# Performance work log

Hardware: AMD Instinct MI355X
Metric: run time of the kernel (lower is better)

Reference implementation:

```python
import jax, jax.numpy as jnp
import numpy as np
from jax import lax

C = 384          # input_dim
HEADS = 12       # num_heads_sp = max(1, 384*1.0 // 30)
HD = 32          # head_dim_sp = 384 // 12
NK = 3           # num_keys (full=True)
ATT_K, ATT_S = 7, 4
UP_K, UP_P = 8, 2   # ConvTranspose2d(kernel=att_stride*2, stride=4, padding=att_stride//2)
EPS = 1e-5
DN = ('NCHW', 'OIHW', 'NCHW')


def _gn(x, g, b):
    # GroupNorm(num_groups=1): normalize over (C,H,W) per sample, per-channel affine
    mu = jnp.mean(x, axis=(1, 2, 3), keepdims=True)
    var = jnp.var(x, axis=(1, 2, 3), keepdims=True)
    return (x - mu) * lax.rsqrt(var + EPS) * g[None, :, None, None] + b[None, :, None, None]


def _pw(x, w):
    # 1x1 conv as einsum; w: [out_ch, in_ch]
    return jnp.einsum('nchw,oc->nohw', x, w)


def _forward(x, dw_w, bn_gamma, bn_beta, bn_mean, bn_var, lnch_gamma, lnch_beta,
             pwise_ch_w, outch_w, outch_b, lnsp_gamma, lnsp_beta,
             pwise_sp_w, outsp_w, outsp_b, up_w, up_b):
    # depthwise strided downsampling conv + BatchNorm (eval mode)
    p = ATT_K // 2
    x_down = lax.conv_general_dilated(x, dw_w, (ATT_S, ATT_S), [(p, p), (p, p)],
                                      dimension_numbers=DN, feature_group_count=C)
    s = bn_gamma * lax.rsqrt(bn_var + EPS)
    x_down = x_down * s[None, :, None, None] + (bn_beta - bn_mean * s)[None, :, None, None]
    N, _, H, W = x_down.shape
    L = H * W
    # --- channel attention: tokens are channels, d_k = H*W ---
    qkv = _pw(_gn(x_down, lnch_gamma, lnch_beta), pwise_ch_w).reshape(N, NK * C, L)
    q, k, v = jnp.split(qkv, NK, axis=1)  # each [N, C, L]
    att = jax.nn.softmax(jnp.einsum('ncl,ndl->ncd', q, k) / jnp.sqrt(jnp.float32(L)), axis=-1)
    vals = jnp.einsum('ncd,ndl->ncl', att, v).reshape(N, C, H, W)
    x_down = x_down + _pw(vals, outch_w) + outch_b[None, :, None, None]
    # --- spatial multi-head attention over the H*W tokens ---
    qkv = _pw(_gn(x_down, lnsp_gamma, lnsp_beta), pwise_sp_w)
    qkv = qkv.reshape(N, HEADS, NK * HD, L).transpose(0, 1, 3, 2)  # [N,h,L,3*hd]
    q, k, v = jnp.split(qkv, NK, axis=-1)  # each [N,h,L,hd]
    att = jax.nn.softmax(jnp.einsum('nhld,nhmd->nhlm', q, k) / jnp.sqrt(jnp.float32(HD)), axis=-1)
    vals = jnp.einsum('nhlm,nhmd->nhld', att, v).transpose(0, 1, 3, 2).reshape(N, HEADS * HD, H, W)
    x_down = x_down + _pw(vals, outsp_w) + outsp_b[None, :, None, None]
    # --- depthwise transposed-conv upsampling (as lhs-dilated conv w/ flipped kernel) ---
    tp = UP_K - 1 - UP_P
    o = lax.conv_general_dilated(x_down, up_w[:, :, ::-1, ::-1], (1, 1), [(tp, tp), (tp, tp)],
                                 lhs_dilation=(ATT_S, ATT_S), dimension_numbers=DN,
                                 feature_group_count=C)
    return x + o + up_b[None, :, None, None]


def setup_inputs():
    key = jax.random.key(0)
    ks = jax.random.split(key, 8)
    w = lambda k, shp: jax.random.normal(k, shp, dtype=jnp.float32) * 0.05
    return {
        'x': jax.random.normal(ks[0], (16, C, 64, 64), dtype=jnp.float32),
        'dw_w': w(ks[1], (C, 1, ATT_K, ATT_K)),
        'bn_gamma': jnp.ones((C,), jnp.float32),
        'bn_beta': jnp.zeros((C,), jnp.float32),
        'bn_mean': jnp.zeros((C,), jnp.float32),
        'bn_var': jnp.ones((C,), jnp.float32),
        'lnch_gamma': jnp.ones((C,), jnp.float32),
        'lnch_beta': jnp.zeros((C,), jnp.float32),
        'pwise_ch_w': w(ks[2], (NK * C, C)),
        'outch_w': w(ks[3], (C, C)),
        'outch_b': jnp.zeros((C,), jnp.float32),
        'lnsp_gamma': jnp.ones((C,), jnp.float32),
        'lnsp_beta': jnp.zeros((C,), jnp.float32),
        'pwise_sp_w': w(ks[4], (NK * HEADS * HD, C)),
        'outsp_w': w(ks[5], (C, HEADS * HD)),
        'outsp_b': jnp.zeros((C,), jnp.float32),
        'up_w': w(ks[6], (C, 1, UP_K, UP_K)),
        'up_b': jnp.zeros((C,), jnp.float32),
    }


def reference(x, dw_w, bn_gamma, bn_beta, bn_mean, bn_var, lnch_gamma, lnch_beta,
              pwise_ch_w, outch_w, outch_b, lnsp_gamma, lnsp_beta,
              pwise_sp_w, outsp_w, outsp_b, up_w, up_b):
    return _forward(x, dw_w, bn_gamma, bn_beta, bn_mean, bn_var, lnch_gamma, lnch_beta,
                    pwise_ch_w, outch_w, outch_b, lnsp_gamma, lnsp_beta,
                    pwise_sp_w, outsp_w, outsp_b, up_w, up_b)
```

## Files before the change

### kernel.cpp

```cpp
#include <hip/hip_runtime.h>
#include <hip/hip_bf16.h>
#include <math.h>

typedef __hip_bfloat16 bf16;

#define NB  16
#define CCH 384
#define LDIM 256

typedef __attribute__((ext_vector_type(8))) short bh8;
typedef __attribute__((ext_vector_type(4))) float fx4;

__device__ __forceinline__ float ldin(const void* p, long i, bool f) {
    if (f) return ((const float*)p)[i];
    return __bfloat162float(((const bf16*)p)[i]);
}
__device__ __forceinline__ float b2f(unsigned short u) {
    union { unsigned short s; bf16 b; } c; c.s = u; return __bfloat162float(c.b);
}
__device__ __forceinline__ unsigned short f2b(float v) {
    bf16 h = __float2bfloat16(v);
    union { bf16 b; unsigned short s; } c; c.b = h; return c.s;
}
__device__ __forceinline__ float fin(float v, float marker) {
    return (v == v && fabsf(v) < 1e30f) ? v : marker;
}

__global__ void k_detect(const unsigned* __restrict__ g, int* __restrict__ flag) {
    if (threadIdx.x == 0) *flag = (*g == 0x3F800000u) ? 1 : 0;
}
__global__ void k_zero(float* __restrict__ p) { p[threadIdx.x] = 0.f; }

__global__ void k_dwconv_bn(const void* __restrict__ x, const void* __restrict__ w,
                            const void* __restrict__ gamma, const void* __restrict__ beta,
                            const void* __restrict__ mean, const void* __restrict__ var,
                            const int* __restrict__ flag, float* __restrict__ xd)
{
    bool f = *flag != 0;
    int c = blockIdx.x, n = blockIdx.y, t = threadIdx.x;
    int i = t >> 4, j = t & 15;
    float s = ldin(gamma, c, f) * rsqrtf(ldin(var, c, f) + 1e-5f);
    float bias = ldin(beta, c, f) - ldin(mean, c, f) * s;
    long xbase = (long)(n * CCH + c) << 12;
    float acc = 0.f;
    #pragma unroll
    for (int a = 0; a < 7; a++) {
        int yy = 4 * i + a - 3;
        if (yy < 0 || yy >= 64) continue;
        #pragma unroll
        for (int b = 0; b < 7; b++) {
            int xx = 4 * j + b - 3;
            if (xx < 0 || xx >= 64) continue;
            acc += ldin(x, xbase + (yy << 6) + xx, f) * ldin(w, c * 49 + a * 7 + b, f);
        }
    }
    xd[((long)(n * CCH + c) << 8) + t] = fin(acc * s + bias, 1.0e4f);
}

__global__ void k_gn_stats(const float* __restrict__ xd, float* __restrict__ stats)
{
    int n = blockIdx.y;
    const float* p = xd + (long)n * (CCH * LDIM) + blockIdx.x * 4096;
    float s = 0.f, s2 = 0.f;
    for (int i = threadIdx.x; i < 4096; i += 256) {
        float v = p[i];
        s += v; s2 += v * v;
    }
    #pragma unroll
    for (int o = 32; o; o >>= 1) { s += __shfl_down(s, o); s2 += __shfl_down(s2, o); }
    __shared__ float sh[4], sh2[4];
    int wid = threadIdx.x >> 6, lane = threadIdx.x & 63;
    if (lane == 0) { sh[wid] = s; sh2[wid] = s2; }
    __syncthreads();
    if (threadIdx.x == 0) {
        atomicAdd(&stats[n * 2],     sh[0] + sh[1] + sh[2] + sh[3]);
        atomicAdd(&stats[n * 2 + 1], sh2[0] + sh2[1] + sh2[2] + sh2[3]);
    }
}

template<bool TB, bool ACCUM, bool AIN, bool GNB>
__global__ __launch_bounds__(256) void k_gemm(
    const void* __restrict__ A, const float* __restrict__ B, float* __restrict__ Cm,
    const void* __restrict__ bias, const int* __restrict__ flag,
    const float* __restrict__ gnstats, const void* __restrict__ gng, const void* __restrict__ gnbt,
    int M, int N, int K, int lda, int ldb, int ldc, long sA, long sB, long sC, float alpha)
{
    bool f = *flag != 0;
    __shared__ unsigned short As[128 * 40];
    __shared__ unsigned short Bs[128 * 40];
    long aoff = (long)blockIdx.z * sA;
    const float* Bb = B + (long)blockIdx.z * sB;
    float* Cb = Cm + (long)blockIdx.z * sC;
    float mu = 0.f, rs = 0.f;
    if (GNB) {
        float S = gnstats[2 * blockIdx.z], S2 = gnstats[2 * blockIdx.z + 1];
        mu = S * (1.f / 98304.f);
        float var = S2 * (1.f / 98304.f) - mu * mu;
        rs = rsqrtf(fmaxf(var, 0.f) + 1e-5f);
    }
    int m0 = blockIdx.y << 7, n0 = blockIdx.x << 7;
    int t = threadIdx.x;
    int w = t >> 6, lane = t & 63;
    int wm = w >> 1, wn = w & 1;
    int lr = lane & 15, lg = lane >> 4;
    int amloc = t >> 3, akloc = (t & 7) << 2;
    int nloc = t & 127, ph = t >> 7;
    fx4 acc[4][4] = {};

    for (int k0 = 0; k0 < K; k0 += 32) {
        #pragma unroll
        for (int p = 0; p < 4; p++) {
            int m = (p << 5) + amloc;
            long ai = aoff + (long)(m0 + m) * lda + k0 + akloc;
            ushort4 uv;
            if (AIN && !f) {
                uv = *(const ushort4*)((const unsigned short*)A + ai);
            } else {
                float4 fv = *(const float4*)((const float*)A + ai);
                uv.x = f2b(fv.x); uv.y = f2b(fv.y); uv.z = f2b(fv.z); uv.w = f2b(fv.w);
            }
            *(ushort4*)&As[m * 40 + akloc] = uv;
        }
        if (!TB) {
            const float* Bp = Bb + n0 + nloc;
            #pragma unroll
            for (int i = 0; i < 8; i++) {
                int p = ph + (i << 1);
                int k = k0 + (p << 1);
                float v0 = Bp[(long)k * ldb];
                float v1 = Bp[(long)(k + 1) * ldb];
                if (GNB) {
                    v0 = (v0 - mu) * rs * ldin(gng, k, f) + ldin(gnbt, k, f);
                    v1 = (v1 - mu) * rs * ldin(gng, k + 1, f) + ldin(gnbt, k + 1, f);
                }
                unsigned int pk = (unsigned)f2b(v0) | ((unsigned)f2b(v1) << 16);
                *(unsigned int*)&Bs[nloc * 40 + (p << 1)] = pk;
            }
        } else {
            #pragma unroll
            for (int p = 0; p < 4; p++) {
                int n = (p << 5) + amloc;
                float4 fv = *(const float4*)(Bb + (long)(n0 + n) * ldb + k0 + akloc);
                ushort4 uv;
                uv.x = f2b(fv.x); uv.y = f2b(fv.y); uv.z = f2b(fv.z); uv.w = f2b(fv.w);
                *(ushort4*)&Bs[n * 40 + akloc] = uv;
            }
        }
        __syncthreads();
        bh8 a[4], b[4];
        #pragma unroll
        for (int mi = 0; mi < 4; mi++)
            a[mi] = *(const bh8*)&As[((wm << 6) + (mi << 4) + lr) * 40 + (lg << 3)];
        #pragma unroll
        for (int nj = 0; nj < 4; nj++)
            b[nj] = *(const bh8*)&Bs[((wn << 6) + (nj << 4) + lr) * 40 + (lg << 3)];
        #pragma unroll
        for (int mi = 0; mi < 4; mi++)
            #pragma unroll
            for (int nj = 0; nj < 4; nj++)
                acc[mi][nj] = __builtin_amdgcn_mfma_f32_16x16x32_bf16(a[mi], b[nj], acc[mi][nj], 0, 0, 0);
        __syncthreads();
    }
    #pragma unroll
    for (int mi = 0; mi < 4; mi++) {
        #pragma unroll
        for (int r = 0; r < 4; r++) {
            int m = m0 + (wm << 6) + (mi << 4) + (lg << 2) + r;
            float bv = bias ? ldin(bias, m, f) : 0.f;
            #pragma unroll
            for (int nj = 0; nj < 4; nj++) {
                int n = n0 + (wn << 6) + (nj << 4) + lr;
                long idx = (long)m * ldc + n;
                float v = alpha * acc[mi][nj][r] + bv;
                if (ACCUM) v += Cb[idx];
                Cb[idx] = fin(v, 4.0e4f);
            }
        }
    }
}

__global__ void k_softmax(float* __restrict__ a, int D)
{
    long row = blockIdx.x;
    float* p = a + row * D;
    int t = threadIdx.x;
    float m = -1e30f;
    for (int i = t; i < D; i += 256) m = fmaxf(m, p[i]);
    #pragma unroll
    for (int o = 32; o; o >>= 1) m = fmaxf(m, __shfl_down(m, o));
    __shared__ float shm[4], shs[4];
    int wid = t >> 6, lane = t & 63;
    if (lane == 0) shm[wid] = m;
    __syncthreads();
    m = fmaxf(fmaxf(shm[0], shm[1]), fmaxf(shm[2], shm[3]));
    float s = 0.f;
    for (int i = t; i < D; i += 256) {
        float e = __expf(p[i] - m);
        p[i] = e;
        s += e;
    }
    #pragma unroll
    for (int o = 32; o; o >>= 1) s += __shfl_down(s, o);
    if (lane == 0) shs[wid] = s;
    __syncthreads();
    float inv = 1.f / (shs[0] + shs[1] + shs[2] + shs[3]);
    for (int i = t; i < D; i += 256) p[i] *= inv;
}

__global__ __launch_bounds__(256) void k_spatt(const float* __restrict__ qkv,
                                               float* __restrict__ vals)
{
    __shared__ float Ks[256 * 36];
    __shared__ float Vs[256 * 36];
    int h = blockIdx.x, n = blockIdx.y, t = threadIdx.x;
    const float* base = qkv + (long)n * 294912 + h * 96 * 256;
    float q[32];
    #pragma unroll
    for (int i = 0; i < 32; i++) {
        q[i] = base[i * 256 + t];
        Ks[t * 36 + i] = base[(32 + i) * 256 + t];
        Vs[t * 36 + i] = base[(64 + i) * 256 + t];
    }
    __syncthreads();
    float o[32] = {};
    float mx = -1e30f, sum = 0.f;
    for (int m = 0; m < 256; m++) {
        float s = 0.f;
        #pragma unroll
        for (int i = 0; i < 8; i++) {
            float4 kv = *(const float4*)&Ks[m * 36 + 4 * i];
            s += q[4*i] * kv.x + q[4*i+1] * kv.y + q[4*i+2] * kv.z + q[4*i+3] * kv.w;
        }
        s *= 0.17677669529663687f;
        if (s > mx) {
            float c = __expf(mx - s);
            sum *= c;
            #pragma unroll
            for (int d = 0; d < 32; d++) o[d] *= c;
            mx = s;
        }
        float p = __expf(s - mx);
        sum += p;
        #pragma unroll
        for (int i = 0; i < 8; i++) {
            float4 vv = *(const float4*)&Vs[m * 36 + 4 * i];
            o[4*i] += p * vv.x; o[4*i+1] += p * vv.y; o[4*i+2] += p * vv.z; o[4*i+3] += p * vv.w;
        }
    }
    float inv = 1.f / sum;
    long ob = (long)n * 98304 + h * 8192;
    #pragma unroll
    for (int d = 0; d < 32; d++) vals[ob + d * 256 + t] = fin(o[d] * inv, 5.0e4f);
}

__global__ void k_upsample(const void* __restrict__ x, const float* __restrict__ xd,
                           const void* __restrict__ w, const void* __restrict__ ub,
                           const int* __restrict__ flag, void* __restrict__ out)
{
    bool f = *flag != 0;
    int c = blockIdx.y, n = blockIdx.z;
    int t = threadIdx.x;
    int p0 = (blockIdx.x * 256 + t) * 4;
    int y = p0 >> 6, xx0 = p0 & 63;
    const float* xdp = xd + ((long)(n * CCH + c) << 8);
    long base = (long)(n * CCH + c) << 12;
    float bias = ldin(ub, c, f);
    float acc[4];
    if (f) {
        #pragma unroll
        for (int e = 0; e < 4; e++) acc[e] = ((const float*)x)[base + p0 + e] + bias;
    } else {
        ushort4 xv = *(const ushort4*)((const unsigned short*)x + base + p0);
        acc[0] = b2f(xv.x) + bias; acc[1] = b2f(xv.y) + bias;
        acc[2] = b2f(xv.z) + bias; acc[3] = b2f(xv.w) + bias;
    }
    int ry = (y + 2) & 3;
    #pragma unroll
    for (int dy = 0; dy < 2; dy++) {
        int ky = ry + 4 * dy;
        int iy = (y + 2 - ky) >> 2;
        if (iy < 0 || iy >= 16) continue;
        #pragma unroll
        for (int e = 0; e < 4; e++) {
            int xxe = xx0 + e;
            int rx = (xxe + 2) & 3;
            #pragma unroll
            for (int dx = 0; dx < 2; dx++) {
                int kx = rx + 4 * dx;
                int ix = (xxe + 2 - kx) >> 2;
                if (ix < 0 || ix >= 16) continue;
                acc[e] += xdp[(iy << 4) + ix] * ldin(w, (c << 6) + (ky << 3) + kx, f);
            }
        }
    }
    if (f) {
        #pragma unroll
        for (int e = 0; e < 4; e++) ((float*)out)[base + p0 + e] = fin(acc[e], 9.0e4f);
    } else {
        ushort4 ov;
        ov.x = f2b(fin(acc[0], 9.0e4f)); ov.y = f2b(fin(acc[1], 9.0e4f));
        ov.z = f2b(fin(acc[2], 9.0e4f)); ov.w = f2b(fin(acc[3], 9.0e4f));
        *(ushort4*)((unsigned short*)out + base + p0) = ov;
    }
}

extern "C" void kernel_launch(void* const* d_in, const int* in_sizes, int n_in,
                              void* d_out, int out_size, void* d_ws, size_t ws_size,
                              hipStream_t stream)
{
    const void* x       = d_in[0];
    const void* dw_w    = d_in[1];
    const void* bn_g    = d_in[2];
    const void* bn_b    = d_in[3];
    const void* bn_m    = d_in[4];
    const void* bn_v    = d_in[5];
    const void* lnch_g  = d_in[6];
    const void* lnch_b  = d_in[7];
    const void* w_ch    = d_in[8];
    const void* outch_w = d_in[9];
    const void* outch_b = d_in[10];
    const void* lnsp_g  = d_in[11];
    const void* lnsp_b  = d_in[12];
    const void* w_sp    = d_in[13];
    const void* outsp_w = d_in[14];
    const void* outsp_b = d_in[15];
    const void* up_w    = d_in[16];
    const void* up_b    = d_in[17];
    float* ws = (float*)d_ws;

    float* xd    = ws;
    float* stats = ws + 1572864;
    int*   flag  = (int*)(ws + 1572864 + 32);

    float* ob   = (float*)d_out;
    float* vals = ob;
    float* qkv  = ob + 1572864;
    float* attb = qkv + 4718592;

    k_detect<<<1, 64, 0, stream>>>((const unsigned*)bn_g, flag);

    k_dwconv_bn<<<dim3(CCH, NB), 256, 0, stream>>>(x, dw_w, bn_g, bn_b, bn_m, bn_v, flag, xd);
    k_zero<<<1, 32, 0, stream>>>(stats);
    k_gn_stats<<<dim3(24, NB), 256, 0, stream>>>(xd, stats);
    k_gemm<false, false, true, true><<<dim3(2, 9, NB), 256, 0, stream>>>(
        w_ch, xd, qkv, nullptr, flag, stats, lnch_g, lnch_b,
        1152, 256, 384, 384, 256, 256, 0L, 98304L, 294912L, 1.f);
    k_gemm<true, false, false, false><<<dim3(3, 3, NB), 256, 0, stream>>>(
        qkv, qkv + 98304, attb, nullptr, flag, nullptr, nullptr, nullptr,
        384, 384, 256, 256, 256, 384, 294912L, 294912L, 147456L, 0.0625f);
    k_softmax<<<NB * 384, 256, 0, stream>>>(attb, 384);
    k_gemm<false, false, false, false><<<dim3(2, 3, NB), 256, 0, stream>>>(
        attb, qkv + 196608, vals, nullptr, flag, nullptr, nullptr, nullptr,
        384, 256, 384, 384, 256, 256, 147456L, 294912L, 98304L, 1.f);
    k_gemm<false, true, true, false><<<dim3(2, 3, NB), 256, 0, stream>>>(
        outch_w, vals, xd, outch_b, flag, nullptr, nullptr, nullptr,
        384, 256, 384, 384, 256, 256, 0L, 98304L, 98304L, 1.f);
    k_zero<<<1, 32, 0, stream>>>(stats);
    k_gn_stats<<<dim3(24, NB), 256, 0, stream>>>(xd, stats);
    k_gemm<false, false, true, true><<<dim3(2, 9, NB), 256, 0, stream>>>(
        w_sp, xd, qkv, nullptr, flag, stats, lnsp_g, lnsp_b,
        1152, 256, 384, 384, 256, 256, 0L, 98304L, 294912L, 1.f);
    k_spatt<<<dim3(12, NB), 256, 0, stream>>>(qkv, vals);
    k_gemm<false, true, true, false><<<dim3(2, 3, NB), 256, 0, stream>>>(
        outsp_w, vals, xd, outsp_b, flag, nullptr, nullptr, nullptr,
        384, 256, 384, 384, 256, 256, 0L, 98304L, 98304L, 1.f);
    k_upsample<<<dim3(4, CCH, NB), 256, 0, stream>>>(x, xd, up_w, up_b, flag, d_out);
}
```

Before: 650.8 us.

## Rewrite spatial attention with bf16 MFMA for QK^T and PV

Replaces the scalar per-thread online-softmax spatial attention with a two-stage matrix-core version. Q, K and V are converted to bf16 in shared memory, QK^T runs on 16x16x32 bf16 MFMAs, and a full-row softmax writes bf16 probabilities to swizzled shared memory. A second MFMA pass computes PV, and the output is transposed through shared memory for coalesced stores. It uses about 150KB of shared memory, which limits it to one block per CU, and lowers the precision of Q, K, V and the probabilities to bf16.

```diff
diff --git a/kernel.cpp b/kernel.cpp
--- a/kernel.cpp
+++ b/kernel.cpp
@@ -207,50 +207,131 @@
     for (int i = t; i < D; i += 256) p[i] *= inv;
 }
 
-__global__ __launch_bounds__(256) void k_spatt(const float* __restrict__ qkv,
-                                               float* __restrict__ vals)
-{
-    __shared__ float Ks[256 * 36];
-    __shared__ float Vs[256 * 36];
+__global__ __launch_bounds__(256, 1) void k_spatt(const float* __restrict__ qkv,
+                                                  float* __restrict__ vals)
+{
+    __shared__ __align__(16) unsigned char smem[152064];
+    unsigned short* Qs = (unsigned short*)smem;
+    unsigned short* Ks = (unsigned short*)(smem + 20480);
+    unsigned char*  Ps = smem;
+    unsigned char*  Vs = smem + 135168;
+    float*          Os = (float*)smem;
+
     int h = blockIdx.x, n = blockIdx.y, t = threadIdx.x;
     const float* base = qkv + (long)n * 294912 + h * 96 * 256;
-    float q[32];
-    #pragma unroll
-    for (int i = 0; i < 32; i++) {
-        q[i] = base[i * 256 + t];
-        Ks[t * 36 + i] = base[(32 + i) * 256 + t];
-        Vs[t * 36 + i] = base[(64 + i) * 256 + t];
-    }
-    __syncthreads();
-    float o[32] = {};
-    float mx = -1e30f, sum = 0.f;
-    for (int m = 0; m < 256; m++) {
-        float s = 0.f;
+
+    {
+        const float* q0 = base + t;
+        const float* k0 = base + 32 * 256 + t;
+        #pragma unroll
+        for (int dp = 0; dp < 16; dp++) {
+            float a0 = q0[(2 * dp) * 256], a1 = q0[(2 * dp + 1) * 256];
+            ((unsigned*)Qs)[t * 20 + dp] = (unsigned)f2b(a0) | ((unsigned)f2b(a1) << 16);
+            float b0 = k0[(2 * dp) * 256], b1 = k0[(2 * dp + 1) * 256];
+            ((unsigned*)Ks)[t * 20 + dp] = (unsigned)f2b(b0) | ((unsigned)f2b(b1) << 16);
+        }
+    }
+    {
+        int d = t >> 3, tok0 = (t & 7) << 5;
+        const float* vp = base + (64 + d) * 256 + tok0;
+        int swz = (d & 7) << 4;
         #pragma unroll
         for (int i = 0; i < 8; i++) {
-            float4 kv = *(const float4*)&Ks[m * 36 + 4 * i];
-            s += q[4*i] * kv.x + q[4*i+1] * kv.y + q[4*i+2] * kv.z + q[4*i+3] * kv.w;
-        }
-        s *= 0.17677669529663687f;
-        if (s > mx) {
-            float c = __expf(mx - s);
-            sum *= c;
-            #pragma unroll
-            for (int d = 0; d < 32; d++) o[d] *= c;
-            mx = s;
-        }
-        float p = __expf(s - mx);
-        sum += p;
-        #pragma unroll
-        for (int i = 0; i < 8; i++) {
-            float4 vv = *(const float4*)&Vs[m * 36 + 4 * i];
-            o[4*i] += p * vv.x; o[4*i+1] += p * vv.y; o[4*i+2] += p * vv.z; o[4*i+3] += p * vv.w;
-        }
-    }
-    float inv = 1.f / sum;
-    long ob = (long)n * 98304 + h * 8192;
-    #pragma unroll
-    for (int d = 0; d < 32; d++) vals[ob + d * 256 + t] = fin(o[d] * inv, 5.0e4f);
+            float4 fv = *(const float4*)(vp + 4 * i);
+            ushort4 uv;
+            uv.x = f2b(fv.x); uv.y = f2b(fv.y); uv.z = f2b(fv.z); uv.w = f2b(fv.w);
+            *(ushort4*)(Vs + d * 528 + ((((tok0 + 4 * i) * 2)) ^ swz)) = uv;
+        }
+    }
+    __syncthreads();
+
+    int lane = t & 63;
+    int lr = lane & 15, lg = lane >> 4;
+    int rbase = (t >> 6) << 6;
+
+    fx4 acc[4][16] = {};
+    {
+        bh8 a[4];
+        #pragma unroll
+        for (int mi = 0; mi < 4; mi++)
+            a[mi] = *(const bh8*)&Qs[(rbase + mi * 16 + lr) * 40 + lg * 8];
+        #pragma unroll
+        for (int nj = 0; nj < 16; nj++) {
+            bh8 b = *(const bh8*)&Ks[(nj * 16 + lr) * 40 + lg * 8];
+            #pragma unroll
+            for (int mi = 0; mi < 4; mi++)
+                acc[mi][nj] = __builtin_amdgcn_mfma_f32_16x16x32_bf16(a[mi], b, acc[mi][nj], 0, 0, 0);
+        }
+    }
+    __syncthreads();
+
+    float inv[4][4];
+    const float scl = 0.17677669529663687f;
+    #pragma unroll
+    for (int mi = 0; mi < 4; mi++) {
+        #pragma unroll
+        for (int r = 0; r < 4; r++) {
+            float s[16];
+            float mx = -1e30f;
+            #pragma unroll
+            for (int nj = 0; nj < 16; nj++) { s[nj] = acc[mi][nj][r] * scl; mx = fmaxf(mx, s[nj]); }
+            #pragma unroll
+            for (int o = 8; o; o >>= 1) mx = fmaxf(mx, __shfl_xor(mx, o));
+            int row = rbase + mi * 16 + lg * 4 + r;
+            int swz = (row & 7) << 4;
+            unsigned char* prow = Ps + row * 528;
+            float sum = 0.f;
+            #pragma unroll
+            for (int nj = 0; nj < 16; nj++) {
+                float p = __expf(s[nj] - mx);
+                sum += p;
+                int col = nj * 16 + lr;
+                *(unsigned short*)(prow + ((col * 2) ^ swz)) = f2b(p);
+            }
+            #pragma unroll
+            for (int o = 8; o; o >>= 1) sum += __shfl_xor(sum, o);
+            inv[mi][r] = 1.f / sum;
+        }
+    }
+
+    fx4 acc2[4][2] = {};
+    #pragma unroll
+    for (int ks = 0; ks < 8; ks++) {
+        bh8 pa[4], vb[2];
+        #pragma unroll
+        for (int mi = 0; mi < 4; mi++) {
+            int row = rbase + mi * 16 + lr;
+            pa[mi] = *(const bh8*)(Ps + row * 528 + ((ks * 64 + lg * 16) ^ ((row & 7) << 4)));
+        }
+        #pragma unroll
+        for (int nj = 0; nj < 2; nj++) {
+            int row = nj * 16 + lr;
+            vb[nj] = *(const bh8*)(Vs + row * 528 + ((ks * 64 + lg * 16) ^ ((row & 7) << 4)));
+        }
+        #pragma unroll
+        for (int mi = 0; mi < 4; mi++)
+            #pragma unroll
+            for (int nj = 0; nj < 2; nj++)
+                acc2[mi][nj] = __builtin_amdgcn_mfma_f32_16x16x32_bf16(pa[mi], vb[nj], acc2[mi][nj], 0, 0, 0);
+    }
+    __syncthreads();
+
+    #pragma unroll
+    for (int mi = 0; mi < 4; mi++)
+        #pragma unroll
+        for (int nj = 0; nj < 2; nj++)
+            #pragma unroll
+            for (int r = 0; r < 4; r++) {
+                int tok = rbase + mi * 16 + lg * 4 + r;
+                int d = nj * 16 + lr;
+                Os[d * 265 + tok] = acc2[mi][nj][r] * inv[mi][r];
+            }
+    __syncthreads();
+
+    long ob = (long)n * 98304 + (long)h * 8192;
+    #pragma unroll
+    for (int d = 0; d < 32; d++)
+        vals[ob + d * 256 + t] = fin(Os[d * 265 + t], 5.0e4f);
 }
 
 __global__ void k_upsample(const void* __restrict__ x, const float* __restrict__ xd,
```

New measurement: 582.8 us. -10.4%, faster.
